# Performance work log

Measured on AMD Instinct MI355X. Metric: run time of the kernel, lower is better.

The kernel has to match this reference:

```python
import jax, jax.numpy as jnp
import numpy as np

DT = 0.05
N_STEPS = 3
DAMP = 0.5
C2 = 1.0  # wave_speed^2


def _shift(u, k):
    # causal shift along T (axis=1): prepend k zeros, drop last k
    T = u.shape[1]
    return jnp.pad(u, ((0, 0), (k, 0), (0, 0)))[:, :T, :]


def dx(u):
    return u - _shift(u, 1)


def dxx(u):
    return u - 2.0 * _shift(u, 1) + _shift(u, 2)


def dxxx(u):
    return u - 3.0 * _shift(u, 1) + 3.0 * _shift(u, 2) - _shift(u, 3)


def dxxxx(u):
    return u - 4.0 * _shift(u, 1) + 6.0 * _shift(u, 2) - 4.0 * _shift(u, 3) + _shift(u, 4)


def _rk4_second_order(u0, rhs, dt, n_steps):
    # state (u, v), u_t = v, v_t = rhs(u, v); zero initial velocity
    u, v = u0, jnp.zeros_like(u0)
    for _ in range(n_steps):
        k1u, k1v = v, rhs(u, v)
        k2u, k2v = v + 0.5 * dt * k1v, rhs(u + 0.5 * dt * k1u, v + 0.5 * dt * k1v)
        k3u, k3v = v + 0.5 * dt * k2v, rhs(u + 0.5 * dt * k2u, v + 0.5 * dt * k2v)
        k4u, k4v = v + dt * k3v, rhs(u + dt * k3u, v + dt * k3v)
        u = u + (dt / 6.0) * (k1u + 2.0 * k2u + 2.0 * k3u + k4u)
        v = v + (dt / 6.0) * (k1v + 2.0 * k2v + 2.0 * k3v + k4v)
    return u


def _rk4_first_order(u0, rhs, dt, n_steps):
    u = u0
    for _ in range(n_steps):
        k1 = rhs(u)
        k2 = rhs(u + 0.5 * dt * k1)
        k3 = rhs(u + 0.5 * dt * k2)
        k4 = rhs(u + dt * k3)
        u = u + (dt / 6.0) * (k1 + 2.0 * k2 + 2.0 * k3 + k4)
    return u


def sine_gordon(u0):
    rhs = lambda u, v: C2 * dxx(u) - jnp.sin(u) - DAMP * v
    return _rk4_second_order(u0, rhs, DT, N_STEPS)


def kdv(u0):
    rhs = lambda u: -6.0 * u * dx(u) - dxxx(u) - DAMP * u
    return _rk4_first_order(u0, rhs, DT * 0.5, N_STEPS)


def heimburg_jackson(u0):
    rhs = lambda u, v: dx((1.0 + u + u * u) * dx(u)) - dxxxx(u) - DAMP * v
    return _rk4_second_order(u0, rhs, DT * 0.5, N_STEPS)


def setup_inputs() -> dict:
    key = jax.random.key(0)
    kx, kw = jax.random.split(key)
    B, T, D = 4, 4096, 1024
    x = jax.random.normal(kx, (B, T, D), dtype=jnp.float32)
    solver_mix = jnp.ones((3,), dtype=jnp.float32) / 3.0
    W = jax.random.normal(kw, (D, D), dtype=jnp.float32) * (1.0 / np.sqrt(D))
    b = jnp.zeros((D,), dtype=jnp.float32)
    return {"x": x, "solver_mix": solver_mix, "W": W, "b": b}


def reference(x, solver_mix, W, b):
    x_field = jnp.tanh(x) * 2.0
    w = jax.nn.softmax(solver_mix, axis=0)
    evolved = (
        w[0] * sine_gordon(x_field)
        + w[1] * kdv(x_field)
        + w[2] * heimburg_jackson(x_field)
    )
    out = jnp.einsum("btd,ed->bte", evolved, W) + b
    return out
```

## Files before the change

kernel.cpp:

```cpp
#include <hip/hip_runtime.h>
#include <hip/hip_bf16.h>


typedef __bf16 bf16x8 __attribute__((ext_vector_type(8)));
typedef __bf16 bf16x4 __attribute__((ext_vector_type(4)));
typedef float  floatx4 __attribute__((ext_vector_type(4)));

#define T_DIM 4096
#define D_DIM 1024
#define NP    16
#define HALO  48
#define NCH   32
#define TINT  (NCH * NP - HALO)
#define NTT   9

__device__ __forceinline__ float sg_rhs(float c, float m1, float m2, float vv) {
  float dxx = fmaf(-2.f, m1, c) + m2;
  return dxx - __sinf(c) - 0.5f * vv;
}
__device__ __forceinline__ float kdv_rhs(float c, float m1, float m2, float m3) {
  float dxu = c - m1;
  float dx3 = fmaf(-3.f, m1, c) + fmaf(3.f, m2, -m3);
  return fmaf(-6.f * c, dxu, -dx3 - 0.5f * c);
}
__device__ __forceinline__ float hj_rhs(float c, float m1, float m2, float m3,
                                        float m4, float vv) {
  float gi = (fmaf(c, c, c) + 1.f) * (c - m1);
  float gm = (fmaf(m1, m1, m1) + 1.f) * (m1 - m2);
  float d4 = fmaf(-4.f, m3, fmaf(6.f, m2, fmaf(-4.f, m1, c))) + m4;
  return (gi - gm) - d4 - 0.5f * vv;
}

#define AT(F, i) (((i) >= 0) ? F[(i)] : hl[4 + (i)])
#define XCHG(F) do { \
    hl[0] = __shfl_up(F[NP - 4], 1, 32); \
    hl[1] = __shfl_up(F[NP - 3], 1, 32); \
    hl[2] = __shfl_up(F[NP - 2], 1, 32); \
    hl[3] = __shfl_up(F[NP - 1], 1, 32); \
  } while (0)

__global__ __launch_bounds__(256, 2)
void pde_kernel(const float* __restrict__ x, const float* __restrict__ mix,
                __bf16* __restrict__ evout) {
  const int tid  = threadIdx.x;
  const int tr   = tid & 31;
  const int dcol = tid >> 5;
  const int yq   = blockIdx.y >> 3;
  const int yr   = blockIdx.y & 7;
  const int d    = (yr * 16 + yq) * 8 + dcol;
  const int b    = blockIdx.z;
  const int t0   = blockIdx.x * TINT;
  const int tb   = t0 - HALO + tr * NP;

  float s0 = mix[0], s1 = mix[1], s2 = mix[2];
  float mxv = fmaxf(s0, fmaxf(s1, s2));
  float e0 = __expf(s0 - mxv), e1 = __expf(s1 - mxv), e2 = __expf(s2 - mxv);
  float inv = 1.f / (e0 + e1 + e2);
  float w0 = e0 * inv, w1 = e1 * inv, w2 = e2 * inv;

  const float* xp = x + ((size_t)b * T_DIM) * D_DIM + d;

  float u0[NP], u[NP], v[NP], ut[NP], vt[NP], au[NP], av[NP], ev[NP], hl[4];

  #pragma unroll
  for (int j = 0; j < NP; ++j) {
    int t = tb + j;
    float xv = (t >= 0 && t < T_DIM) ? xp[(size_t)t * D_DIM] : 0.f;
    float xc = fminf(fmaxf(xv, -9.f), 9.f);
    float ex = __expf(2.f * xc);
    u0[j] = 2.f - 4.f * __builtin_amdgcn_rcpf(ex + 1.f);
  }

  {
    const float dt = 0.05f, h = 0.025f, w6 = dt * (1.f / 6.f);
    #pragma unroll
    for (int j = 0; j < NP; ++j) { u[j] = u0[j]; v[j] = 0.f; }
    #pragma unroll 1
    for (int s = 0; s < 3; ++s) {
      XCHG(u);
      #pragma unroll
      for (int i = NP - 1; i >= 0; --i) {
        float k = sg_rhs(u[i], AT(u, i - 1), AT(u, i - 2), v[i]);
        au[i] = v[i]; av[i] = k;
        ut[i] = fmaf(h, v[i], u[i]);
        vt[i] = fmaf(h, k, v[i]);
      }
      XCHG(ut);
      #pragma unroll
      for (int i = NP - 1; i >= 0; --i) {
        float k = sg_rhs(ut[i], AT(ut, i - 1), AT(ut, i - 2), vt[i]);
        au[i] = fmaf(2.f, vt[i], au[i]); av[i] = fmaf(2.f, k, av[i]);
        float nu = fmaf(h, vt[i], u[i]);
        vt[i] = fmaf(h, k, v[i]);
        ut[i] = nu;
      }
      XCHG(ut);
      #pragma unroll
      for (int i = NP - 1; i >= 0; --i) {
        float k = sg_rhs(ut[i], AT(ut, i - 1), AT(ut, i - 2), vt[i]);
        au[i] = fmaf(2.f, vt[i], au[i]); av[i] = fmaf(2.f, k, av[i]);
        float nu = fmaf(dt, vt[i], u[i]);
        vt[i] = fmaf(dt, k, v[i]);
        ut[i] = nu;
      }
      XCHG(ut);
      #pragma unroll
      for (int i = NP - 1; i >= 0; --i) {
        float k = sg_rhs(ut[i], AT(ut, i - 1), AT(ut, i - 2), vt[i]);
        au[i] += vt[i]; av[i] += k;
        u[i] = fmaf(w6, au[i], u[i]);
        v[i] = fmaf(w6, av[i], v[i]);
      }
    }
    #pragma unroll
    for (int j = 0; j < NP; ++j) ev[j] = w0 * u[j];
  }

  {
    const float dt = 0.025f, h = 0.0125f, w6 = dt * (1.f / 6.f);
    #pragma unroll
    for (int j = 0; j < NP; ++j) u[j] = u0[j];
    #pragma unroll 1
    for (int s = 0; s < 3; ++s) {
      XCHG(u);
      #pragma unroll
      for (int i = NP - 1; i >= 0; --i) {
        float k = kdv_rhs(u[i], AT(u, i - 1), AT(u, i - 2), AT(u, i - 3));
        au[i] = k;
        ut[i] = fmaf(h, k, u[i]);
      }
      XCHG(ut);
      #pragma unroll
      for (int i = NP - 1; i >= 0; --i) {
        float k = kdv_rhs(ut[i], AT(ut, i - 1), AT(ut, i - 2), AT(ut, i - 3));
        au[i] = fmaf(2.f, k, au[i]);
        ut[i] = fmaf(h, k, u[i]);
      }
      XCHG(ut);
      #pragma unroll
      for (int i = NP - 1; i >= 0; --i) {
        float k = kdv_rhs(ut[i], AT(ut, i - 1), AT(ut, i - 2), AT(ut, i - 3));
        au[i] = fmaf(2.f, k, au[i]);
        ut[i] = fmaf(dt, k, u[i]);
      }
      XCHG(ut);
      #pragma unroll
      for (int i = NP - 1; i >= 0; --i) {
        float k = kdv_rhs(ut[i], AT(ut, i - 1), AT(ut, i - 2), AT(ut, i - 3));
        u[i] = fmaf(w6, au[i] + k, u[i]);
      }
    }
    #pragma unroll
    for (int j = 0; j < NP; ++j) ev[j] = fmaf(w1, u[j], ev[j]);
  }

  {
    const float dt = 0.025f, h = 0.0125f, w6 = dt * (1.f / 6.f);
    #pragma unroll
    for (int j = 0; j < NP; ++j) { u[j] = u0[j]; v[j] = 0.f; }
    #pragma unroll 1
    for (int s = 0; s < 3; ++s) {
      XCHG(u);
      #pragma unroll
      for (int i = NP - 1; i >= 0; --i) {
        float k = hj_rhs(u[i], AT(u, i - 1), AT(u, i - 2), AT(u, i - 3),
                         AT(u, i - 4), v[i]);
        au[i] = v[i]; av[i] = k;
        ut[i] = fmaf(h, v[i], u[i]);
        vt[i] = fmaf(h, k, v[i]);
      }
      XCHG(ut);
      #pragma unroll
      for (int i = NP - 1; i >= 0; --i) {
        float k = hj_rhs(ut[i], AT(ut, i - 1), AT(ut, i - 2), AT(ut, i - 3),
                         AT(ut, i - 4), vt[i]);
        au[i] = fmaf(2.f, vt[i], au[i]); av[i] = fmaf(2.f, k, av[i]);
        float nu = fmaf(h, vt[i], u[i]);
        vt[i] = fmaf(h, k, v[i]);
        ut[i] = nu;
      }
      XCHG(ut);
      #pragma unroll
      for (int i = NP - 1; i >= 0; --i) {
        float k = hj_rhs(ut[i], AT(ut, i - 1), AT(ut, i - 2), AT(ut, i - 3),
                         AT(ut, i - 4), vt[i]);
        au[i] = fmaf(2.f, vt[i], au[i]); av[i] = fmaf(2.f, k, av[i]);
        float nu = fmaf(dt, vt[i], u[i]);
        vt[i] = fmaf(dt, k, v[i]);
        ut[i] = nu;
      }
      XCHG(ut);
      #pragma unroll
      for (int i = NP - 1; i >= 0; --i) {
        float k = hj_rhs(ut[i], AT(ut, i - 1), AT(ut, i - 2), AT(ut, i - 3),
                         AT(ut, i - 4), vt[i]);
        au[i] += vt[i]; av[i] += k;
        u[i] = fmaf(w6, au[i], u[i]);
        v[i] = fmaf(w6, av[i], v[i]);
      }
    }
    #pragma unroll
    for (int j = 0; j < NP; ++j) ev[j] = fmaf(w2, u[j], ev[j]);
  }

  if (tr >= 3) {
    #pragma unroll
    for (int j = 0; j < NP; ++j) {
      int t = tb + j;
      if (t < T_DIM)
        evout[((size_t)(b * T_DIM + t)) * D_DIM + d] = (__bf16)ev[j];
    }
  }
}

__global__ __launch_bounds__(256)
void convert_w(const float* __restrict__ W, __bf16* __restrict__ Wb) {
  int i = blockIdx.x * 256 + threadIdx.x;
  float4 f = ((const float4*)W)[i];
  bf16x4 o = {(__bf16)f.x, (__bf16)f.y, (__bf16)f.z, (__bf16)f.w};
  ((bf16x4*)Wb)[i] = o;
}

#define GK   1024

__global__ __launch_bounds__(256, 2)
void gemm_kernel(const __bf16* __restrict__ A, const __bf16* __restrict__ Bw,
                 const float* __restrict__ bias, float* __restrict__ out) {
  __shared__ __align__(16) __bf16 As[128 * 64];
  __shared__ __align__(16) __bf16 Bs[256 * 64];

  const int tid  = threadIdx.x;
  const int lane = tid & 63;
  const int wid  = tid >> 6;
  const int m0   = blockIdx.x * 128;
  const int n0   = blockIdx.y * 256;
  const int wm   = (wid >> 1) * 64;
  const int wn   = (wid & 1) * 128;
  const int l15  = lane & 15;
  const int quad = lane >> 4;

  const int sr  = lane >> 3;
  const int skc = (lane & 7) ^ sr;

  floatx4 acc[4][8] = {};

  for (int kt = 0; kt < GK; kt += 64) {
    __syncthreads();
    #pragma unroll
    for (int p = 0; p < 4; ++p) {
      int rowblk = wid * 32 + p * 8;
      const __bf16* ga = A + (size_t)(m0 + rowblk + sr) * GK + kt + skc * 8;
      __builtin_amdgcn_global_load_lds((const uint32_t*)ga,
                                       (uint32_t*)&As[rowblk * 64], 16, 0, 0);
    }
    #pragma unroll
    for (int p = 0; p < 8; ++p) {
      int rowblk = wid * 64 + p * 8;
      const __bf16* gb = Bw + (size_t)(n0 + rowblk + sr) * GK + kt + skc * 8;
      __builtin_amdgcn_global_load_lds((const uint32_t*)gb,
                                       (uint32_t*)&Bs[rowblk * 64], 16, 0, 0);
    }
    __syncthreads();
    #pragma unroll
    for (int c = 0; c < 2; ++c) {
      bf16x8 af[4], bfr[8];
      int kcg = c * 4 + quad;
      #pragma unroll
      for (int i = 0; i < 4; ++i) {
        int ra = wm + i * 16 + l15;
        af[i] = *(const bf16x8*)(&As[ra * 64 + ((kcg ^ (ra & 7)) * 8)]);
      }
      #pragma unroll
      for (int j = 0; j < 8; ++j) {
        int rb = wn + j * 16 + l15;
        bfr[j] = *(const bf16x8*)(&Bs[rb * 64 + ((kcg ^ (rb & 7)) * 8)]);
      }
      #pragma unroll
      for (int i = 0; i < 4; ++i)
        #pragma unroll
        for (int j = 0; j < 8; ++j)
          acc[i][j] = __builtin_amdgcn_mfma_f32_16x16x32_bf16(
              af[i], bfr[j], acc[i][j], 0, 0, 0);
    }
  }

  #pragma unroll
  for (int j = 0; j < 8; ++j) {
    int n = n0 + wn + j * 16 + l15;
    float bv = bias[n];
    #pragma unroll
    for (int i = 0; i < 4; ++i) {
      int mb = m0 + wm + i * 16 + quad * 4;
      #pragma unroll
      for (int r = 0; r < 4; ++r)
        out[(size_t)(mb + r) * 1024 + n] = acc[i][j][r] + bv;
    }
  }
}

extern "C" void kernel_launch(void* const* d_in, const int* in_sizes, int n_in,
                              void* d_out, int out_size, void* d_ws, size_t ws_size,
                              hipStream_t stream) {
  const float* x    = (const float*)d_in[0];
  const float* mix  = (const float*)d_in[1];
  const float* W    = (const float*)d_in[2];
  const float* bias = (const float*)d_in[3];
  float* out = (float*)d_out;

  __bf16* ev = (__bf16*)d_ws;
  __bf16* Wb = (__bf16*)((char*)d_ws + (size_t)32 * 1024 * 1024);

  convert_w<<<dim3((D_DIM * D_DIM / 4) / 256), 256, 0, stream>>>(W, Wb);
  pde_kernel<<<dim3(NTT, 128, 4), 256, 0, stream>>>(x, mix, ev);
  gemm_kernel<<<dim3(16384 / 128, 1024 / 256), 256, 0, stream>>>(ev, Wb, bias, out);
}
```

Before: 328.1 us.

## Enlarge GEMM tile to 256x256 with 8 waves and double-buffered LDS

The GEMM now uses 256x256 output tiles computed by 512 threads (8 waves, each 128x64). The A and B tiles go into two LDS buffers, so the next K-slice's global-to-LDS loads are issued while the current slice is multiplied, and one barrier per iteration replaces two. This aims to hide memory latency and raise arithmetic intensity. In exchange, LDS use grows to 128KB per block, occupancy drops to one block per CU, and the grid shrinks to 256 blocks.

```diff
diff --git a/kernel.cpp b/kernel.cpp
--- a/kernel.cpp
+++ b/kernel.cpp
@@ -223,73 +223,83 @@
 
 #define GK   1024
 
-__global__ __launch_bounds__(256, 2)
+__global__ __launch_bounds__(512, 1)
 void gemm_kernel(const __bf16* __restrict__ A, const __bf16* __restrict__ Bw,
                  const float* __restrict__ bias, float* __restrict__ out) {
-  __shared__ __align__(16) __bf16 As[128 * 64];
-  __shared__ __align__(16) __bf16 Bs[256 * 64];
+  __shared__ __align__(16) __bf16 As[2][256 * 64];
+  __shared__ __align__(16) __bf16 Bs[2][256 * 64];
 
   const int tid  = threadIdx.x;
   const int lane = tid & 63;
   const int wid  = tid >> 6;
-  const int m0   = blockIdx.x * 128;
+  const int m0   = blockIdx.x * 256;
   const int n0   = blockIdx.y * 256;
-  const int wm   = (wid >> 1) * 64;
-  const int wn   = (wid & 1) * 128;
+  const int wm   = (wid >> 2) * 128;
+  const int wn   = (wid & 3) * 64;
   const int l15  = lane & 15;
   const int quad = lane >> 4;
 
   const int sr  = lane >> 3;
   const int skc = (lane & 7) ^ sr;
 
-  floatx4 acc[4][8] = {};
-
-  for (int kt = 0; kt < GK; kt += 64) {
-    __syncthreads();
-    #pragma unroll
-    for (int p = 0; p < 4; ++p) {
-      int rowblk = wid * 32 + p * 8;
-      const __bf16* ga = A + (size_t)(m0 + rowblk + sr) * GK + kt + skc * 8;
-      __builtin_amdgcn_global_load_lds((const uint32_t*)ga,
-                                       (uint32_t*)&As[rowblk * 64], 16, 0, 0);
-    }
-    #pragma unroll
-    for (int p = 0; p < 8; ++p) {
-      int rowblk = wid * 64 + p * 8;
-      const __bf16* gb = Bw + (size_t)(n0 + rowblk + sr) * GK + kt + skc * 8;
-      __builtin_amdgcn_global_load_lds((const uint32_t*)gb,
-                                       (uint32_t*)&Bs[rowblk * 64], 16, 0, 0);
-    }
-    __syncthreads();
+  const __bf16* aBase = A  + (size_t)(m0 + wid * 32 + sr) * GK + skc * 8;
+  const __bf16* bBase = Bw + (size_t)(n0 + wid * 32 + sr) * GK + skc * 8;
+
+#define STAGE(buf, kt) do {                                                   \
+    _Pragma("unroll")                                                         \
+    for (int p = 0; p < 4; ++p)                                               \
+      __builtin_amdgcn_global_load_lds(                                       \
+          (const uint32_t*)(aBase + (size_t)(p * 8) * GK + (kt)),             \
+          (uint32_t*)&As[buf][(wid * 32 + p * 8) * 64], 16, 0, 0);            \
+    _Pragma("unroll")                                                         \
+    for (int p = 0; p < 4; ++p)                                               \
+      __builtin_amdgcn_global_load_lds(                                       \
+          (const uint32_t*)(bBase + (size_t)(p * 8) * GK + (kt)),             \
+          (uint32_t*)&Bs[buf][(wid * 32 + p * 8) * 64], 16, 0, 0);            \
+  } while (0)
+
+  floatx4 acc[8][4] = {};
+
+  STAGE(0, 0);
+  __syncthreads();
+
+  int cur = 0;
+  for (int kt = 64; kt <= GK; kt += 64) {
+    if (kt < GK) STAGE(cur ^ 1, kt);
+    const __bf16* as = As[cur];
+    const __bf16* bs = Bs[cur];
     #pragma unroll
     for (int c = 0; c < 2; ++c) {
-      bf16x8 af[4], bfr[8];
+      bf16x8 af[8], bfr[4];
       int kcg = c * 4 + quad;
       #pragma unroll
-      for (int i = 0; i < 4; ++i) {
+      for (int i = 0; i < 8; ++i) {
         int ra = wm + i * 16 + l15;
-        af[i] = *(const bf16x8*)(&As[ra * 64 + ((kcg ^ (ra & 7)) * 8)]);
-      }
-      #pragma unroll
-      for (int j = 0; j < 8; ++j) {
+        af[i] = *(const bf16x8*)(&as[ra * 64 + ((kcg ^ (ra & 7)) * 8)]);
+      }
+      #pragma unroll
+      for (int j = 0; j < 4; ++j) {
         int rb = wn + j * 16 + l15;
-        bfr[j] = *(const bf16x8*)(&Bs[rb * 64 + ((kcg ^ (rb & 7)) * 8)]);
-      }
-      #pragma unroll
-      for (int i = 0; i < 4; ++i)
+        bfr[j] = *(const bf16x8*)(&bs[rb * 64 + ((kcg ^ (rb & 7)) * 8)]);
+      }
+      #pragma unroll
+      for (int i = 0; i < 8; ++i)
         #pragma unroll
-        for (int j = 0; j < 8; ++j)
+        for (int j = 0; j < 4; ++j)
           acc[i][j] = __builtin_amdgcn_mfma_f32_16x16x32_bf16(
               af[i], bfr[j], acc[i][j], 0, 0, 0);
     }
-  }
+    __syncthreads();
+    cur ^= 1;
+  }
+#undef STAGE
 
   #pragma unroll
-  for (int j = 0; j < 8; ++j) {
+  for (int j = 0; j < 4; ++j) {
     int n = n0 + wn + j * 16 + l15;
     float bv = bias[n];
     #pragma unroll
-    for (int i = 0; i < 4; ++i) {
+    for (int i = 0; i < 8; ++i) {
       int mb = m0 + wm + i * 16 + quad * 4;
       #pragma unroll
       for (int r = 0; r < 4; ++r)
@@ -312,5 +322,5 @@
 
   convert_w<<<dim3((D_DIM * D_DIM / 4) / 256), 256, 0, stream>>>(W, Wb);
   pde_kernel<<<dim3(NTT, 128, 4), 256, 0, stream>>>(x, mix, ev);
-  gemm_kernel<<<dim3(16384 / 128, 1024 / 256), 256, 0, stream>>>(ev, Wb, bias, out);
-}
+  gemm_kernel<<<dim3(16384 / 256, 1024 / 256), 512, 0, stream>>>(ev, Wb, bias, out);
+}
```

New measurement: 324.4 us. Within noise of the previous version (-1.2%).
